# Optimization experiments

Measured on AMD Instinct MI355X. Metric: run time of the kernel, lower is better.

## Reference

```python
import jax, jax.numpy as jnp
import numpy as np

OBS_LEN = 16          # observation_len in SnapKV
KERNEL = 5            # AvgPool1d kernel_size
MAX_CACHE_LEN = 2048  # max_cache_length


def _avg_pool1d_nopad(x, k=KERNEL):
    """AvgPool1d(kernel=k, stride=1, padding=k//2, count_include_pad=False) over last axis."""
    S = x.shape[-1]
    pad = k // 2
    zero = jnp.zeros(x.shape[:-1] + (1,), x.dtype)
    c0 = jnp.concatenate([zero, jnp.cumsum(x, axis=-1)], axis=-1)  # [..., S+1]
    i = jnp.arange(S)
    hi = jnp.minimum(i + pad + 1, S)  # exclusive window end
    lo = jnp.maximum(i - pad, 0)      # inclusive window start
    wsum = jnp.take(c0, hi, axis=-1) - jnp.take(c0, lo, axis=-1)
    return wsum / (hi - lo).astype(x.dtype)


def setup_inputs() -> dict:
    key = jax.random.key(0)
    k1, k2, k3 = jax.random.split(key, 3)
    B, H, Q, S, D = 1, 32, 64, 8192, 128
    # realistic attention weights: softmax over key axis
    attn = jax.nn.softmax(jax.random.normal(k1, (B, H, Q, S), jnp.float32), axis=-1)
    k_val = jax.random.normal(k2, (B, H, S, D), jnp.float32)
    v_val = jax.random.normal(k3, (B, H, S, D), jnp.float32)
    input_pos = jnp.arange(S, dtype=jnp.int32)
    return {"attn": attn, "k_val": k_val, "v_val": v_val, "input_pos": input_pos}


def reference(attn, k_val, v_val, input_pos):
    # ---- SnapKV prompt compression (_compress_prompt_w_snapkv) ----
    # priority: mean attention received by each key over the last OBS_LEN queries
    priority = attn[:, :, -OBS_LEN:, :].mean(axis=2)          # [B, H, S]
    attn_history = priority                                    # pre-pooling copy
    pooled = _avg_pool1d_nopad(priority)                       # [B, H, S]
    pooled = pooled.at[:, :, -OBS_LEN:].set(1.0)               # always keep observation window
    _, keep_idxs = jax.lax.top_k(pooled, MAX_CACHE_LEN)        # [B, H, L]
    keep_idxs = jnp.sort(keep_idxs, axis=-1)
    attn_history_c = jnp.take_along_axis(attn_history, keep_idxs, axis=-1)  # [B, H, L]
    idx4 = keep_idxs[..., None]                                # [B, H, L, 1]
    k_compressed = jnp.take_along_axis(k_val, idx4, axis=2)    # [B, H, L, D]
    v_compressed = jnp.take_along_axis(v_val, idx4, axis=2)    # [B, H, L, D]
    # ---- cache fill (update / fill_headwise): compressed tokens fill the whole cache ----
    k_cache = k_compressed
    v_cache = v_compressed
    pos = keep_idxs[0].astype(jnp.int32)                       # head-specific positions, [H, L]
    return k_cache, v_cache, attn_history_c, pos
```

## Files before the change

### kernel.cpp

```cpp
#include <hip/hip_runtime.h>

#define H 32
#define Q 64
#define S 8192
#define D 128
#define OBS 16
#define L 2048

__global__ __launch_bounds__(1024) void k_select(const float* __restrict__ attn,
                                                 int* __restrict__ keep,
                                                 float* __restrict__ hist_out,
                                                 float* __restrict__ pos_out) {
    __shared__ float pr[S];
    __shared__ int wtot[16];
    __shared__ int rcount[32];
    const int h = blockIdx.x;
    const int tid = threadIdx.x;
    const int lane = tid & 63, wid = tid >> 6;

    if (tid < 32) rcount[tid] = 0;

    {
        const float* abase = attn + ((size_t)(h * Q + (Q - OBS))) * S;
        float4 a0 = make_float4(0.f, 0.f, 0.f, 0.f);
        float4 a1 = make_float4(0.f, 0.f, 0.f, 0.f);
#pragma unroll
        for (int q = 0; q < OBS; ++q) {
            const float4* row = (const float4*)(abase + (size_t)q * S);
            float4 v0 = row[tid];
            float4 v1 = row[tid + 1024];
            a0.x += v0.x; a0.y += v0.y; a0.z += v0.z; a0.w += v0.w;
            a1.x += v1.x; a1.y += v1.y; a1.z += v1.z; a1.w += v1.w;
        }
        const float inv = 1.0f / (float)OBS;
        a0.x *= inv; a0.y *= inv; a0.z *= inv; a0.w *= inv;
        a1.x *= inv; a1.y *= inv; a1.z *= inv; a1.w *= inv;
        ((float4*)pr)[tid] = a0;
        ((float4*)pr)[tid + 1024] = a1;
    }
    __syncthreads();

    unsigned key[8];
    const int s0 = tid * 8;
    {
        float w[12];
#pragma unroll
        for (int i = 0; i < 12; ++i) {
            int idx = s0 - 2 + i;
            w[i] = (idx >= 0 && idx < S) ? pr[idx] : 0.f;
        }
#pragma unroll
        for (int j = 0; j < 8; ++j) {
            int s = s0 + j;
            float pooled;
            if (s >= S - OBS) {
                pooled = 1.0f;
            } else {
                int lo = s - 2; if (lo < 0) lo = 0;
                int hi = s + 3;
                float sum = 0.f;
                for (int i = lo; i < hi; ++i) sum += w[i - s0 + 2];
                pooled = sum / (float)(hi - lo);
            }
            key[j] = __float_as_uint(pooled);
        }
    }

    unsigned prefix = 0;
    int k = L;
    for (int b = 31; b >= 0; --b) {
        const unsigned bit = 1u << b;
        const unsigned want = prefix | bit;
        const unsigned mask = ~(bit - 1u);
        int cnt = 0;
#pragma unroll
        for (int j = 0; j < 8; ++j) cnt += ((key[j] & mask) == want) ? 1 : 0;
#pragma unroll
        for (int off = 32; off > 0; off >>= 1) cnt += __shfl_down(cnt, off);
        if (lane == 0) atomicAdd(&rcount[b], cnt);
        __syncthreads();
        int total = rcount[b];
        if (total >= k) prefix = want; else k -= total;
    }
    const unsigned T = prefix;
    const int needed_eq = k;

    int gt = 0, eq = 0;
#pragma unroll
    for (int j = 0; j < 8; ++j) {
        gt += (key[j] > T) ? 1 : 0;
        eq += (key[j] == T) ? 1 : 0;
    }
    int packed = (gt << 16) | eq;
    int v = packed;
#pragma unroll
    for (int off = 1; off < 64; off <<= 1) {
        int u = __shfl_up(v, off);
        if (lane >= off) v += u;
    }
    if (lane == 63) wtot[wid] = v;
    __syncthreads();
    int base = 0;
    for (int w = 0; w < wid; ++w) base += wtot[w];
    int excl = base + v - packed;
    int gt_before = excl >> 16;
    int eq_before = excl & 0xffff;

    {
        int g = gt_before, e = eq_before;
#pragma unroll
        for (int j = 0; j < 8; ++j) {
            bool isgt = key[j] > T;
            bool iseq = key[j] == T;
            bool sel = isgt || (iseq && (e < needed_eq));
            if (sel) {
                int s = s0 + j;
                int rank = g + (e < needed_eq ? e : needed_eq);
                size_t o = (size_t)h * L + rank;
                keep[o] = s;
                pos_out[o] = (float)s;
                hist_out[o] = pr[s];
            }
            g += isgt ? 1 : 0;
            e += iseq ? 1 : 0;
        }
    }
}

__global__ void k_gather(const float* __restrict__ kv_k, const float* __restrict__ kv_v,
                         const int* __restrict__ keep, float* __restrict__ out) {
    const int tid = threadIdx.x;
    const int idx = blockIdx.x * 8 + (tid >> 5);
    const int lane = tid & 31;
    const int h = idx >> 11;
    const int s = keep[idx];
    const float4* srcK = (const float4*)(kv_k + (size_t)(h * S + s) * D);
    const float4* srcV = (const float4*)(kv_v + (size_t)(h * S + s) * D);
    float4* dstK = (float4*)(out + (size_t)idx * D);
    float4* dstV = (float4*)(out + ((size_t)H * L + idx) * D);
    dstK[lane] = srcK[lane];
    dstV[lane] = srcV[lane];
}

extern "C" void kernel_launch(void* const* d_in, const int* in_sizes, int n_in,
                              void* d_out, int out_size, void* d_ws, size_t ws_size,
                              hipStream_t stream) {
    const float* attn = (const float*)d_in[0];
    const float* k_val = (const float*)d_in[1];
    const float* v_val = (const float*)d_in[2];

    float* out = (float*)d_out;
    float* hist = out + (size_t)2 * H * L * D;
    float* pos = hist + (size_t)H * L;

    int* keep = (int*)d_ws;

    k_select<<<H, 1024, 0, stream>>>(attn, keep, hist, pos);
    k_gather<<<(H * L) / 8, 256, 0, stream>>>(k_val, v_val, keep, out);
}
```

Measured before the change: 313.4 us.

## Split priority reduction into wide kernel and use 8-bit radix select

Moves the mean over the last 16 query rows into a separate kernel launched across 256 blocks, so that reading the attention rows no longer depends on only 32 blocks. The top-k threshold search changes from a 32-step bitwise radix select, each step with a block barrier, to 4 passes of 8-bit histogram radix select using per-wave shared histograms. The cost is an extra launch and a round trip of the priority array through global memory.

```diff
diff --git a/kernel.cpp b/kernel.cpp
--- a/kernel.cpp
+++ b/kernel.cpp
@@ -7,36 +7,39 @@
 #define OBS 16
 #define L 2048
 
-__global__ __launch_bounds__(1024) void k_select(const float* __restrict__ attn,
+__global__ void k_priority(const float* __restrict__ attn, float* __restrict__ prio) {
+    int gid = blockIdx.x;
+    int h = gid >> 3;
+    int chunk = gid & 7;
+    int s4 = chunk * 1024 + threadIdx.x * 4;
+    const float4* base = (const float4*)(attn + ((size_t)(h * Q + (Q - OBS)) * S + s4));
+    float4 acc = make_float4(0.f, 0.f, 0.f, 0.f);
+#pragma unroll
+    for (int qq = 0; qq < OBS; ++qq) {
+        float4 v = base[qq * (S / 4)];
+        acc.x += v.x; acc.y += v.y; acc.z += v.z; acc.w += v.w;
+    }
+    const float inv = 1.0f / (float)OBS;
+    acc.x *= inv; acc.y *= inv; acc.z *= inv; acc.w *= inv;
+    *((float4*)(prio + (size_t)h * S + s4)) = acc;
+}
+
+__global__ __launch_bounds__(1024) void k_select(const float* __restrict__ prio,
                                                  int* __restrict__ keep,
                                                  float* __restrict__ hist_out,
                                                  float* __restrict__ pos_out) {
     __shared__ float pr[S];
+    __shared__ int whist[16][257];
     __shared__ int wtot[16];
-    __shared__ int rcount[32];
+    __shared__ int res_byte, res_k;
     const int h = blockIdx.x;
     const int tid = threadIdx.x;
     const int lane = tid & 63, wid = tid >> 6;
 
-    if (tid < 32) rcount[tid] = 0;
-
     {
-        const float* abase = attn + ((size_t)(h * Q + (Q - OBS))) * S;
-        float4 a0 = make_float4(0.f, 0.f, 0.f, 0.f);
-        float4 a1 = make_float4(0.f, 0.f, 0.f, 0.f);
-#pragma unroll
-        for (int q = 0; q < OBS; ++q) {
-            const float4* row = (const float4*)(abase + (size_t)q * S);
-            float4 v0 = row[tid];
-            float4 v1 = row[tid + 1024];
-            a0.x += v0.x; a0.y += v0.y; a0.z += v0.z; a0.w += v0.w;
-            a1.x += v1.x; a1.y += v1.y; a1.z += v1.z; a1.w += v1.w;
-        }
-        const float inv = 1.0f / (float)OBS;
-        a0.x *= inv; a0.y *= inv; a0.z *= inv; a0.w *= inv;
-        a1.x *= inv; a1.y *= inv; a1.z *= inv; a1.w *= inv;
-        ((float4*)pr)[tid] = a0;
-        ((float4*)pr)[tid + 1024] = a1;
+        const float4* src = (const float4*)(prio + (size_t)h * S);
+        ((float4*)pr)[tid] = src[tid];
+        ((float4*)pr)[tid + 1024] = src[tid + 1024];
     }
     __syncthreads();
 
@@ -68,19 +71,58 @@
 
     unsigned prefix = 0;
     int k = L;
-    for (int b = 31; b >= 0; --b) {
-        const unsigned bit = 1u << b;
-        const unsigned want = prefix | bit;
-        const unsigned mask = ~(bit - 1u);
-        int cnt = 0;
-#pragma unroll
-        for (int j = 0; j < 8; ++j) cnt += ((key[j] & mask) == want) ? 1 : 0;
-#pragma unroll
-        for (int off = 32; off > 0; off >>= 1) cnt += __shfl_down(cnt, off);
-        if (lane == 0) atomicAdd(&rcount[b], cnt);
+    for (int pass = 3; pass >= 0; --pass) {
+        for (int i = tid; i < 16 * 257; i += 1024) ((int*)whist)[i] = 0;
         __syncthreads();
-        int total = rcount[b];
-        if (total >= k) prefix = want; else k -= total;
+        const int shift = pass * 8;
+        {
+            int cur = -1, run = 0;
+#pragma unroll
+            for (int j = 0; j < 8; ++j) {
+                unsigned kk = key[j];
+                bool match = (pass == 3) || ((kk >> (shift + 8)) == prefix);
+                int b = match ? (int)((kk >> shift) & 255u) : -1;
+                if (b != cur) {
+                    if (cur >= 0) atomicAdd(&whist[wid][cur], run);
+                    cur = b; run = 1;
+                } else {
+                    run++;
+                }
+            }
+            if (cur >= 0) atomicAdd(&whist[wid][cur], run);
+        }
+        __syncthreads();
+        if (wid == 0) {
+            int b0 = 0, b1 = 0, b2 = 0, b3 = 0;
+            const int bb0 = 4 * lane;
+#pragma unroll
+            for (int w = 0; w < 16; ++w) {
+                b0 += whist[w][bb0 + 0];
+                b1 += whist[w][bb0 + 1];
+                b2 += whist[w][bb0 + 2];
+                b3 += whist[w][bb0 + 3];
+            }
+            int lane_sum = b0 + b1 + b2 + b3;
+            int suffix = lane_sum;
+#pragma unroll
+            for (int off = 1; off < 64; off <<= 1) {
+                int u = __shfl_down(suffix, off);
+                if (lane + off < 64) suffix += u;
+            }
+            int suffix_next = suffix - lane_sum;
+            if (suffix >= k && suffix_next < k) {
+                int bins[4] = {b0, b1, b2, b3};
+                int cum = suffix_next;
+                for (int bb = 3; bb >= 0; --bb) {
+                    int nc = cum + bins[bb];
+                    if (nc >= k) { res_byte = bb0 + bb; res_k = k - cum; break; }
+                    cum = nc;
+                }
+            }
+        }
+        __syncthreads();
+        prefix = (prefix << 8) | (unsigned)res_byte;
+        k = res_k;
     }
     const unsigned T = prefix;
     const int needed_eq = k;
@@ -153,8 +195,10 @@
     float* hist = out + (size_t)2 * H * L * D;
     float* pos = hist + (size_t)H * L;
 
-    int* keep = (int*)d_ws;
-
-    k_select<<<H, 1024, 0, stream>>>(attn, keep, hist, pos);
+    float* prio = (float*)d_ws;
+    int* keep = (int*)((char*)d_ws + (size_t)H * S * sizeof(float));
+
+    k_priority<<<256, 256, 0, stream>>>(attn, prio);
+    k_select<<<H, 1024, 0, stream>>>(prio, keep, hist, pos);
     k_gather<<<(H * L) / 8, 256, 0, stream>>>(k_val, v_val, keep, out);
 }
```

Result: faster. 297.2 us (-5.2%).
